# Performance work log

Hardware: AMD Instinct MI355X
Metric: run time of the kernel (lower is better)

Reference implementation:

```python
import jax, jax.numpy as jnp
import numpy as np

N_NODES = 50000
N_EDGES = 800000
F_IN = 128
HEADS = 2
F_OUT = 128  # out_channels == nfeat for the residual


def setup_inputs() -> dict:
    key = jax.random.key(0)
    k_x, k_e, k_u, k_c, k_w, k_b = jax.random.split(key, 6)
    x = jax.random.normal(k_x, (N_NODES, F_IN), dtype=jnp.float32)
    edge_index = jax.random.randint(k_e, (2, N_EDGES), 0, N_NODES, dtype=jnp.int64)
    # FeaStConv params (PyG init: normal(mean=0, std=0.1))
    u = 0.1 * jax.random.normal(k_u, (F_IN, HEADS), dtype=jnp.float32)       # attention proj
    c = 0.1 * jax.random.normal(k_c, (HEADS,), dtype=jnp.float32)            # attention bias
    w = 0.1 * jax.random.normal(k_w, (F_IN, HEADS * F_OUT), dtype=jnp.float32)  # lin weight
    bias = 0.1 * jax.random.normal(k_b, (F_OUT,), dtype=jnp.float32)
    return {"x": x, "edge_index": edge_index, "u": u, "c": c, "w": w, "bias": bias}


def _feast_conv(x, edge_index, u, c, w, bias):
    n = x.shape[0]
    # add self loops (PyG FeaStConv default add_self_loops=True)
    loops = jnp.arange(n, dtype=edge_index.dtype)
    src = jnp.concatenate([edge_index[0], loops])  # j (source / message sender)
    dst = jnp.concatenate([edge_index[1], loops])  # i (target / aggregator)
    e = src.shape[0]
    # per-edge attention over heads: q = softmax(u^T (x_j - x_i) + c)
    xi = x[dst]                                   # [E, F_in]
    xj = x[src]                                   # [E, F_in]
    q = jax.nn.softmax((xj - xi) @ u + c, axis=-1)  # [E, H]
    # per-node linear, then gather per edge
    xw = (x @ w).reshape(n, HEADS, F_OUT)         # [N, H, F_out]
    msg = jnp.einsum('eh,ehf->ef', q, xw[src])    # [E, F_out]
    # mean aggregation at destinations
    agg = jax.ops.segment_sum(msg, dst, num_segments=n)
    cnt = jax.ops.segment_sum(jnp.ones((e,), x.dtype), dst, num_segments=n)
    return agg / jnp.maximum(cnt, 1.0)[:, None] + bias


def reference(x, edge_index, u, c, w, bias):
    # module forward: x + relu(FeaStConv(x, edge_index))
    return x + jax.nn.relu(_feast_conv(x, edge_index, u, c, w, bias))
```

## Files before the change

kernel.cpp:

```cpp
#include <hip/hip_runtime.h>
#include <hip/hip_bf16.h>

constexpr int N_NODES = 50000;
constexpr int N_EDGES = 800000;
constexpr int F_IN    = 128;
constexpr int F_OUT   = 128;
constexpr int HEADS   = 2;
constexpr int WCOLS   = HEADS * F_OUT;
constexpr int WE_ROWS = 272;
constexpr int SEG     = 64;

typedef __attribute__((ext_vector_type(8))) short  bf16x8;
typedef __attribute__((ext_vector_type(4))) float  f32x4;
typedef __attribute__((ext_vector_type(2))) float  f32x2;
typedef __attribute__((ext_vector_type(4))) unsigned int u32x4;

static __device__ __forceinline__ unsigned short f32_to_bf16_bits(float f) {
    unsigned int u = __float_as_uint(f);
    u += 0x7fffu + ((u >> 16) & 1u);
    return (unsigned short)(u >> 16);
}

static __device__ __forceinline__ bf16x8 pack_bf16x8(const f32x4 a, const f32x4 b) {
    u32x4 p;
    asm("v_cvt_pk_bf16_f32 %0, %1, %2" : "=v"(p[0]) : "v"(a[0]), "v"(a[1]));
    asm("v_cvt_pk_bf16_f32 %0, %1, %2" : "=v"(p[1]) : "v"(a[2]), "v"(a[3]));
    asm("v_cvt_pk_bf16_f32 %0, %1, %2" : "=v"(p[2]) : "v"(b[0]), "v"(b[1]));
    asm("v_cvt_pk_bf16_f32 %0, %1, %2" : "=v"(p[3]) : "v"(b[2]), "v"(b[3]));
    return __builtin_bit_cast(bf16x8, p);
}

__global__ __launch_bounds__(256) void wt_cnt_kernel(const float* __restrict__ w,
                                                     const float* __restrict__ u,
                                                     unsigned short* __restrict__ wTe,
                                                     int* __restrict__ cnt) {
    const int tid = blockIdx.x * 256 + threadIdx.x;
    if (tid < WE_ROWS * F_IN) {
        const int r = tid >> 7;
        const int k = tid & 127;
        float v;
        if (r < WCOLS)            v = w[k * WCOLS + r];
        else if (r < WCOLS + 2)   v = u[k * HEADS + (r - WCOLS)];
        else                      v = 0.f;
        wTe[tid] = f32_to_bf16_bits(v);
    }
    if (tid < N_NODES) cnt[tid] = 0;
}

constexpr int RG = 4;

__global__ __launch_bounds__(256) void proj_kernel(const float* __restrict__ x,
                                                   const unsigned short* __restrict__ wTe,
                                                   unsigned char* __restrict__ xwf,
                                                   float2* __restrict__ s_tab) {
    const int lane = threadIdx.x & 63;
    const int wv   = threadIdx.x >> 6;
    const int n0   = blockIdx.x * (16 * RG);
    const int l15  = lane & 15;
    const int kg   = lane >> 4;

    f32x4 acc[RG][4];
    f32x4 acc4[RG];
#pragma unroll
    for (int rg = 0; rg < RG; ++rg) {
        acc4[rg] = (f32x4){0.f, 0.f, 0.f, 0.f};
#pragma unroll
        for (int t = 0; t < 4; ++t) acc[rg][t] = acc4[rg];
    }

#pragma unroll
    for (int ks = 0; ks < 4; ++ks) {
        bf16x8 xf[RG];
#pragma unroll
        for (int rg = 0; rg < RG; ++rg) {
            const int row = min(n0 + rg * 16 + l15, N_NODES - 1);
            const float* xp = x + (size_t)row * F_IN + ks * 32 + kg * 8;
            const f32x4 xa = *(const f32x4*)xp;
            const f32x4 xb = *(const f32x4*)(xp + 4);
            xf[rg] = pack_bf16x8(xa, xb);
        }

        const unsigned short* wbase = wTe + (size_t)(wv * 64 + l15) * F_IN + ks * 32 + kg * 8;
        const bf16x8 wf0 = *(const bf16x8*)(wbase);
        const bf16x8 wf1 = *(const bf16x8*)(wbase + 16 * F_IN);
        const bf16x8 wf2 = *(const bf16x8*)(wbase + 32 * F_IN);
        const bf16x8 wf3 = *(const bf16x8*)(wbase + 48 * F_IN);

#pragma unroll
        for (int rg = 0; rg < RG; ++rg) {
            acc[rg][0] = __builtin_amdgcn_mfma_f32_16x16x32_bf16(wf0, xf[rg], acc[rg][0], 0, 0, 0);
            acc[rg][1] = __builtin_amdgcn_mfma_f32_16x16x32_bf16(wf1, xf[rg], acc[rg][1], 0, 0, 0);
            acc[rg][2] = __builtin_amdgcn_mfma_f32_16x16x32_bf16(wf2, xf[rg], acc[rg][2], 0, 0, 0);
            acc[rg][3] = __builtin_amdgcn_mfma_f32_16x16x32_bf16(wf3, xf[rg], acc[rg][3], 0, 0, 0);
        }
        if (wv == 3) {
            const unsigned short* ubase = wTe + (size_t)(256 + l15) * F_IN + ks * 32 + kg * 8;
            const bf16x8 uf = *(const bf16x8*)(ubase);
#pragma unroll
            for (int rg = 0; rg < RG; ++rg)
                acc4[rg] = __builtin_amdgcn_mfma_f32_16x16x32_bf16(uf, xf[rg], acc4[rg], 0, 0, 0);
        }
    }

#pragma unroll
    for (int rg = 0; rg < RG; ++rg) {
        const int row = n0 + rg * 16 + l15;
        if (row < N_NODES) {
            unsigned char* orow = xwf + (size_t)row * WCOLS + wv * 64 + kg * 4;
#pragma unroll
            for (int t = 0; t < 4; ++t) {
                unsigned int pk = 0;
                pk = __builtin_amdgcn_cvt_pk_fp8_f32(acc[rg][t][0], acc[rg][t][1], pk, false);
                pk = __builtin_amdgcn_cvt_pk_fp8_f32(acc[rg][t][2], acc[rg][t][3], pk, true);
                *(unsigned int*)(orow + t * 16) = pk;
            }
            if (wv == 3 && kg == 0) {
                s_tab[row] = make_float2(acc4[rg][0], acc4[rg][1]);
            }
        }
    }
}

constexpr int EPT    = 4;
constexpr int CHUNK  = 256 * EPT;
constexpr int NCHUNK = (N_EDGES + CHUNK - 1) / CHUNK;
constexpr int NGROUP = 8;
constexpr int DRANGE = N_NODES / NGROUP;

__global__ __launch_bounds__(256) void scatter_kernel(const int* __restrict__ ei,
                                                      const float2* __restrict__ s,
                                                      const float* __restrict__ c,
                                                      int* __restrict__ cnt,
                                                      unsigned int* __restrict__ rec) {
    const int g     = blockIdx.x & (NGROUP - 1);
    const int chunk = blockIdx.x >> 3;
    const int dlo   = g * DRANGE;
    const int dhi   = dlo + DRANGE;
    const int base  = chunk * CHUNK + threadIdx.x;
    const float c0 = c[0], c1 = c[1];

    int  dstv[EPT];
    bool keep[EPT];
#pragma unroll
    for (int k = 0; k < EPT; ++k) {
        const int e = base + k * 256;
        const int ec = (e < N_EDGES) ? e : 0;
        dstv[k] = ei[N_EDGES + ec];
        keep[k] = (e < N_EDGES) && (dstv[k] >= dlo) && (dstv[k] < dhi);
    }
    int pos[EPT], srcv[EPT];
#pragma unroll
    for (int k = 0; k < EPT; ++k) {
        pos[k]  = keep[k] ? atomicAdd(&cnt[dstv[k]], 1) : 0;
        const int e = base + k * 256;
        srcv[k] = keep[k] ? ei[e] : 0;
    }
#pragma unroll
    for (int k = 0; k < EPT; ++k) {
        if (keep[k]) {
            const float2 ss = s[srcv[k]];
            const float2 sd = s[dstv[k]];
            const float l0 = ss.x - sd.x + c0;
            const float l1 = ss.y - sd.y + c1;
            const float m  = fmaxf(l0, l1);
            const float e0 = __expf(l0 - m);
            const float e1 = __expf(l1 - m);
            const float q0 = e0 / (e0 + e1);
            const unsigned int q16 = (unsigned int)(q0 * 65535.0f + 0.5f);
            const int p = min(pos[k], SEG - 1);
            rec[(size_t)dstv[k] * SEG + p] = (q16 << 16) | (unsigned int)srcv[k];
        }
    }
}

#define AGG_SLOT(K, A)                                                        \
    {                                                                         \
        const unsigned int r = rp[j + K];                                     \
        const unsigned int g = *(const unsigned int*)(gb + (size_t)(r & 0xffffu) * WCOLS); \
        const float q = fmaf(qsign, (float)(r >> 16) * (1.0f/65535.0f), qbase);\
        const f32x2 glo = __builtin_amdgcn_cvt_pk_f32_fp8(g, false);          \
        const f32x2 ghi = __builtin_amdgcn_cvt_pk_f32_fp8(g, true);           \
        A.x = fmaf(q, glo[0], A.x);                                           \
        A.y = fmaf(q, glo[1], A.y);                                           \
        A.z = fmaf(q, ghi[0], A.z);                                           \
        A.w = fmaf(q, ghi[1], A.w);                                           \
    }

__global__ __launch_bounds__(256) void agg_kernel(const float* __restrict__ x,
                                                  const float* __restrict__ bias,
                                                  const float* __restrict__ c,
                                                  const unsigned char* __restrict__ xwf,
                                                  const unsigned int* __restrict__ rec,
                                                  const int* __restrict__ cnt,
                                                  float* __restrict__ out) {
    const int lane = threadIdx.x & 63;
    const int half = lane >> 5;
    const int l5   = lane & 31;
    const int n    = blockIdx.x * 4 + (threadIdx.x >> 6);
    if (n >= N_NODES) return;
    const int m_cnt = min(cnt[n], SEG);
    const int deg   = m_cnt + 1;
    const unsigned int* rp = rec + (size_t)n * SEG;

    const float qbase = half ? 1.0f : 0.0f;
    const float qsign = half ? -1.0f : 1.0f;
    const unsigned char* gb = xwf + half * F_OUT + 4 * l5;

    const float c0 = c[0], c1 = c[1];
    const float mm = fmaxf(c0, c1);
    const float se0 = __expf(c0 - mm);
    const float se1 = __expf(c1 - mm);
    const float qs = fmaf(qsign, se0 / (se0 + se1), qbase);
    const unsigned int gsv = *(const unsigned int*)(gb + (size_t)n * WCOLS);
    const f32x2 slo = __builtin_amdgcn_cvt_pk_f32_fp8(gsv, false);
    const f32x2 shi = __builtin_amdgcn_cvt_pk_f32_fp8(gsv, true);
    float4 a0, a1 = {0.f,0.f,0.f,0.f}, a2 = a1, a3 = a1;
    a0.x = qs * slo[0];
    a0.y = qs * slo[1];
    a0.z = qs * shi[0];
    a0.w = qs * shi[1];

    int j = 0;
    for (; j + 4 <= m_cnt; j += 4) {
        AGG_SLOT(0, a0) AGG_SLOT(1, a1) AGG_SLOT(2, a2) AGG_SLOT(3, a3)
    }
    for (; j < m_cnt; ++j) {
        AGG_SLOT(0, a0)
    }
    float4 t;
    t.x = (a0.x + a1.x) + (a2.x + a3.x);
    t.y = (a0.y + a1.y) + (a2.y + a3.y);
    t.z = (a0.z + a1.z) + (a2.z + a3.z);
    t.w = (a0.w + a1.w) + (a2.w + a3.w);
    t.x += __shfl_xor(t.x, 32, 64);
    t.y += __shfl_xor(t.y, 32, 64);
    t.z += __shfl_xor(t.z, 32, 64);
    t.w += __shfl_xor(t.w, 32, 64);
    if (half == 0) {
        const float inv = 1.0f / (float)deg;
        const float4 bv = *(const float4*)(bias + 4 * l5);
        const float4 xv = *(const float4*)(x + (size_t)n * F_IN + 4 * l5);
        float4 r;
        r.x = xv.x + fmaxf(fmaf(t.x, inv, bv.x), 0.f);
        r.y = xv.y + fmaxf(fmaf(t.y, inv, bv.y), 0.f);
        r.z = xv.z + fmaxf(fmaf(t.z, inv, bv.z), 0.f);
        r.w = xv.w + fmaxf(fmaf(t.w, inv, bv.w), 0.f);
        *(float4*)(out + (size_t)n * F_OUT + 4 * l5) = r;
    }
}

extern "C" void kernel_launch(void* const* d_in, const int* in_sizes, int n_in,
                              void* d_out, int out_size, void* d_ws, size_t ws_size,
                              hipStream_t stream) {
    const float* x    = (const float*)d_in[0];
    const int*   ei   = (const int*)  d_in[1];
    const float* u    = (const float*)d_in[2];
    const float* c    = (const float*)d_in[3];
    const float* w    = (const float*)d_in[4];
    const float* bias = (const float*)d_in[5];
    float* out = (float*)d_out;

    char* p = (char*)d_ws;
    unsigned char* xwf = (unsigned char*)p;    p += (size_t)N_NODES * WCOLS;
    float2* s_tab  = (float2*)p;               p += (size_t)N_NODES * sizeof(float2);
    int*    cnt    = (int*)p;                  p += (size_t)N_NODES * sizeof(int);
    unsigned short* wTe = (unsigned short*)p;  p += (size_t)WE_ROWS * F_IN * sizeof(unsigned short);
    unsigned int* rec = (unsigned int*)p;

    wt_cnt_kernel<<<(N_NODES + 255) / 256, 256, 0, stream>>>(w, u, wTe, cnt);

    proj_kernel<<<(N_NODES + 16 * RG - 1) / (16 * RG), 256, 0, stream>>>(x, wTe, xwf, s_tab);

    scatter_kernel<<<NGROUP * NCHUNK, 256, 0, stream>>>(ei, s_tab, c, cnt, rec);

    agg_kernel<<<(N_NODES + 3) / 4, 256, 0, stream>>>(x, bias, c, xwf, rec, cnt, out);
}
```

Before: 123.8 us.

## Split edge scatter into bucket-by-destination-group pass and per-group CSR fill pass

The old scatter kernel re-read the destination indices eight times, once per destination group, and did per-node atomics and record writes in a single pass. It now runs two passes. The first reads each edge once, computes the attention weight, and appends (record, dst) into one of eight global buckets using block-local shared atomics plus one global atomic per group. The second walks each bucket and does the per-node atomics and record writes, so those writes stay inside one destination range per block and get better L2 locality. This adds an extra kernel launch and an intermediate bucket round trip of 8 bytes per edge, and the bucket capacity is fixed at GCAP.

```diff
diff --git a/kernel.cpp b/kernel.cpp
--- a/kernel.cpp
+++ b/kernel.cpp
@@ -33,7 +33,8 @@
 __global__ __launch_bounds__(256) void wt_cnt_kernel(const float* __restrict__ w,
                                                      const float* __restrict__ u,
                                                      unsigned short* __restrict__ wTe,
-                                                     int* __restrict__ cnt) {
+                                                     int* __restrict__ cnt,
+                                                     int* __restrict__ gcount) {
     const int tid = blockIdx.x * 256 + threadIdx.x;
     if (tid < WE_ROWS * F_IN) {
         const int r = tid >> 7;
@@ -45,6 +46,7 @@
         wTe[tid] = f32_to_bf16_bits(v);
     }
     if (tid < N_NODES) cnt[tid] = 0;
+    if (tid < 8) gcount[tid] = 0;
 }
 
 constexpr int RG = 4;
@@ -126,38 +128,41 @@
 constexpr int NCHUNK = (N_EDGES + CHUNK - 1) / CHUNK;
 constexpr int NGROUP = 8;
 constexpr int DRANGE = N_NODES / NGROUP;
-
-__global__ __launch_bounds__(256) void scatter_kernel(const int* __restrict__ ei,
-                                                      const float2* __restrict__ s,
-                                                      const float* __restrict__ c,
-                                                      int* __restrict__ cnt,
-                                                      unsigned int* __restrict__ rec) {
-    const int g     = blockIdx.x & (NGROUP - 1);
-    const int chunk = blockIdx.x >> 3;
-    const int dlo   = g * DRANGE;
-    const int dhi   = dlo + DRANGE;
-    const int base  = chunk * CHUNK + threadIdx.x;
+constexpr int GCAP   = 131072;
+
+__global__ __launch_bounds__(256) void scatterA_kernel(const int* __restrict__ ei,
+                                                       const float2* __restrict__ s,
+                                                       const float* __restrict__ c,
+                                                       int* __restrict__ gcount,
+                                                       uint2* __restrict__ bucket) {
+    __shared__ int lcnt[NGROUP];
+    __shared__ int lbase[NGROUP];
+    const int tid = threadIdx.x;
+    if (tid < NGROUP) lcnt[tid] = 0;
+    __syncthreads();
+
+    const int base = blockIdx.x * CHUNK + tid;
     const float c0 = c[0], c1 = c[1];
 
-    int  dstv[EPT];
-    bool keep[EPT];
+    int  srcv[EPT], dstv[EPT], gv[EPT], lpos[EPT];
+    bool val[EPT];
 #pragma unroll
     for (int k = 0; k < EPT; ++k) {
-        const int e = base + k * 256;
-        const int ec = (e < N_EDGES) ? e : 0;
+        const int e  = base + k * 256;
+        val[k] = (e < N_EDGES);
+        const int ec = val[k] ? e : 0;
+        srcv[k] = ei[ec];
         dstv[k] = ei[N_EDGES + ec];
-        keep[k] = (e < N_EDGES) && (dstv[k] >= dlo) && (dstv[k] < dhi);
-    }
-    int pos[EPT], srcv[EPT];
+        gv[k]   = dstv[k] / DRANGE;
+        lpos[k] = val[k] ? atomicAdd(&lcnt[gv[k]], 1) : 0;
+    }
+    __syncthreads();
+    if (tid < NGROUP) lbase[tid] = atomicAdd(&gcount[tid], lcnt[tid]);
+    __syncthreads();
+
 #pragma unroll
     for (int k = 0; k < EPT; ++k) {
-        pos[k]  = keep[k] ? atomicAdd(&cnt[dstv[k]], 1) : 0;
-        const int e = base + k * 256;
-        srcv[k] = keep[k] ? ei[e] : 0;
-    }
-#pragma unroll
-    for (int k = 0; k < EPT; ++k) {
-        if (keep[k]) {
+        if (val[k]) {
             const float2 ss = s[srcv[k]];
             const float2 sd = s[dstv[k]];
             const float l0 = ss.x - sd.x + c0;
@@ -167,9 +172,27 @@
             const float e1 = __expf(l1 - m);
             const float q0 = e0 / (e0 + e1);
             const unsigned int q16 = (unsigned int)(q0 * 65535.0f + 0.5f);
-            const int p = min(pos[k], SEG - 1);
-            rec[(size_t)dstv[k] * SEG + p] = (q16 << 16) | (unsigned int)srcv[k];
-        }
+            const int idx = min(lbase[gv[k]] + lpos[k], GCAP - 1);
+            bucket[(size_t)gv[k] * GCAP + idx] =
+                make_uint2((q16 << 16) | (unsigned int)srcv[k], (unsigned int)dstv[k]);
+        }
+    }
+}
+
+constexpr int NB_B = 96;
+
+__global__ __launch_bounds__(256) void scatterB_kernel(const uint2* __restrict__ bucket,
+                                                       const int* __restrict__ gcount,
+                                                       int* __restrict__ cnt,
+                                                       unsigned int* __restrict__ rec) {
+    const int g = blockIdx.x & (NGROUP - 1);
+    const int n = min(gcount[g], GCAP);
+    const uint2* bp = bucket + (size_t)g * GCAP;
+    for (int i = (blockIdx.x >> 3) * 256 + threadIdx.x; i < n; i += NB_B * 256) {
+        const uint2 ent = bp[i];
+        const int dst = (int)ent.y;
+        const int pos = atomicAdd(&cnt[dst], 1);
+        rec[(size_t)dst * SEG + min(pos, SEG - 1)] = ent.x;
     }
 }
 
@@ -264,14 +287,18 @@
     unsigned char* xwf = (unsigned char*)p;    p += (size_t)N_NODES * WCOLS;
     float2* s_tab  = (float2*)p;               p += (size_t)N_NODES * sizeof(float2);
     int*    cnt    = (int*)p;                  p += (size_t)N_NODES * sizeof(int);
+    int*    gcount = (int*)p;                  p += 256;
     unsigned short* wTe = (unsigned short*)p;  p += (size_t)WE_ROWS * F_IN * sizeof(unsigned short);
-    unsigned int* rec = (unsigned int*)p;
-
-    wt_cnt_kernel<<<(N_NODES + 255) / 256, 256, 0, stream>>>(w, u, wTe, cnt);
+    unsigned int* rec = (unsigned int*)p;      p += (size_t)N_NODES * SEG * sizeof(unsigned int);
+    uint2*  bucket = (uint2*)p;
+
+    wt_cnt_kernel<<<(N_NODES + 255) / 256, 256, 0, stream>>>(w, u, wTe, cnt, gcount);
 
     proj_kernel<<<(N_NODES + 16 * RG - 1) / (16 * RG), 256, 0, stream>>>(x, wTe, xwf, s_tab);
 
-    scatter_kernel<<<NGROUP * NCHUNK, 256, 0, stream>>>(ei, s_tab, c, cnt, rec);
+    scatterA_kernel<<<NCHUNK, 256, 0, stream>>>(ei, s_tab, c, gcount, bucket);
+
+    scatterB_kernel<<<NGROUP * NB_B, 256, 0, stream>>>(bucket, gcount, cnt, rec);
 
     agg_kernel<<<(N_NODES + 3) / 4, 256, 0, stream>>>(x, bias, c, xwf, rec, cnt, out);
 }
```

Result: slower. 136.2 us (+10.0%).
